# Kernel tuning notes

Measured on AMD Instinct MI355X. Metric: run time of the kernel, lower is better.

The kernel has to match this reference:

```python
import jax, jax.numpy as jnp
import numpy as np

K = 4      # number of per-slot Linear layers (self.k)
H = 512    # hidden_dim
B = 4      # branching factor at every tree level (B >= K -> no padded slots)
T = 1024   # number of trees (roots)
D = 3      # pooled tree levels (= idx_matrix.shape[1] - 2)
N0 = T * B ** D  # 65536 leaves


def _make_level(n_in):
    """Replicates the torch order_matrix / pooling construction for groups of size B.
    order[m, i] = group_base + (pos_in_group + m) % B, then +1 for the zero pad row.
    seg[i] = group id (torch.repeat_interleave of counts)."""
    i = np.arange(n_in)
    base = (i // B) * B
    pos = i % B
    m = np.arange(K)[:, None]
    order = base[None, :] + (pos[None, :] + m) % B + 1  # [K, n_in], all valid since B >= K
    seg = i // B
    return order.astype(np.int32), seg.astype(np.int32)


def setup_inputs() -> dict:
    key = jax.random.key(0)
    ks = jax.random.split(key, 5)
    x = jax.random.normal(ks[0], (N0, H), jnp.float32)
    node_idx = jnp.arange(N0, dtype=jnp.int32)  # idx_matrix[:, -1]
    o1, s1 = _make_level(N0)
    o2, s2 = _make_level(N0 // B)
    o3, s3 = _make_level(N0 // B // B)
    Wz = jax.random.normal(ks[1], (K, H, H), jnp.float32) / np.sqrt(H)   # k slot Linears
    bz = jax.random.normal(ks[2], (K, H), jnp.float32) * 0.02
    Wzf = jax.random.normal(ks[3], (H, H), jnp.float32) / np.sqrt(H)     # z_final_layer
    bzf = jax.random.normal(ks[4], (H,), jnp.float32) * 0.02
    return dict(x=x, Wz=Wz, bz=bz, Wzf=Wzf, bzf=bzf, node_idx=node_idx,
                order1=jnp.asarray(o1), order2=jnp.asarray(o2), order3=jnp.asarray(o3),
                seg1=jnp.asarray(s1), seg2=jnp.asarray(s2), seg3=jnp.asarray(s3))


def _tree_layer(data, order, seg, num_seg, Wz, bz, Wzf, bzf):
    # prepend zero row so padded entries (order == 0) gather zeros
    padded = jnp.concatenate([jnp.zeros((1, data.shape[-1]), data.dtype), data], axis=0)
    emb = padded[order]                                    # [K, N, H] gather
    emb = jnp.einsum('knh,kjh->nkj', emb, Wz) + bz[None]   # per-slot Linear (x @ W.T + b)
    emb = jnp.where((order.T == 0)[..., None], jnp.zeros((), emb.dtype), emb)  # mask padded slots
    emb = emb.sum(axis=1)                                  # sum over K slots -> [N, H]
    emb = emb @ Wzf.T + bzf                                # z_final_layer
    return jax.ops.segment_sum(emb, seg, num_segments=num_seg)  # global_add_pool


def reference(x, Wz, bz, Wzf, bzf, node_idx, order1, order2, order3, seg1, seg2, seg3):
    data = x[node_idx]
    for order, seg in ((order1, seg1), (order2, seg2), (order3, seg3)):
        data = _tree_layer(data, order, seg, order.shape[1] // B, Wz, bz, Wzf, bzf)
    return data  # [T, H]
```

## Files before the change

kernel.cpp:

```cpp
#include <hip/hip_runtime.h>


#define HD 512

typedef __attribute__((ext_vector_type(8))) short bf16x8;
typedef __attribute__((ext_vector_type(4))) float f32x4;

struct __align__(16) MfmaSmem {
    unsigned short Ah[64][40];
    unsigned short Al[64][40];
    unsigned short Bh[64][40];
    unsigned short Bl[64][40];
};

__device__ __forceinline__ void split8(const float4& v0, const float4& v1,
                                       bf16x8& hv, bf16x8& lv) {
    float f[8] = {v0.x, v0.y, v0.z, v0.w, v1.x, v1.y, v1.z, v1.w};
    #pragma unroll
    for (int i = 0; i < 8; ++i) {
        unsigned u = __float_as_uint(f[i]);
        hv[i] = (short)(u >> 16);
        float hi = __uint_as_float(u & 0xFFFF0000u);
        lv[i] = (short)(__float_as_uint(f[i] - hi) >> 16);
    }
}

template<bool BIAS>
__device__ __forceinline__
void mfma_gemm(const float* __restrict__ A, const float* __restrict__ Bt,
               float* __restrict__ C, const float* __restrict__ bias,
               float bscale, int i0, int j0, MfmaSmem& sm) {
    const int t = threadIdx.x;
    const int sr = t >> 2, sk = (t & 3) << 3;
    const int lane = t & 63, w = t >> 6;
    const int fm = lane & 15, fq = (lane >> 4) << 3;

    const float* ap = &A[(size_t)(i0 + sr) * HD + sk];
    const float* bp = &Bt[(size_t)(j0 + sr) * HD + sk];
    float4 a0 = *(const float4*)ap, a1 = *(const float4*)(ap + 4);
    float4 b0 = *(const float4*)bp, b1 = *(const float4*)(bp + 4);

    f32x4 acc[4] = {};

    for (int it = 0; it < 16; ++it) {
        __syncthreads();
        bf16x8 hv, lv;
        split8(a0, a1, hv, lv);
        *(bf16x8*)&sm.Ah[sr][sk] = hv;
        *(bf16x8*)&sm.Al[sr][sk] = lv;
        split8(b0, b1, hv, lv);
        *(bf16x8*)&sm.Bh[sr][sk] = hv;
        *(bf16x8*)&sm.Bl[sr][sk] = lv;
        __syncthreads();

        if (it < 15) {
            const int k0n = (it + 1) << 5;
            a0 = *(const float4*)(ap + k0n);
            a1 = *(const float4*)(ap + k0n + 4);
            b0 = *(const float4*)(bp + k0n);
            b1 = *(const float4*)(bp + k0n + 4);
        }

        bf16x8 ah = *(const bf16x8*)&sm.Ah[(w << 4) + fm][fq];
        bf16x8 al = *(const bf16x8*)&sm.Al[(w << 4) + fm][fq];
        #pragma unroll
        for (int ct = 0; ct < 4; ++ct) {
            bf16x8 bh = *(const bf16x8*)&sm.Bh[(ct << 4) + fm][fq];
            bf16x8 bl = *(const bf16x8*)&sm.Bl[(ct << 4) + fm][fq];
            acc[ct] = __builtin_amdgcn_mfma_f32_16x16x32_bf16(ah, bh, acc[ct], 0, 0, 0);
            acc[ct] = __builtin_amdgcn_mfma_f32_16x16x32_bf16(ah, bl, acc[ct], 0, 0, 0);
            acc[ct] = __builtin_amdgcn_mfma_f32_16x16x32_bf16(al, bh, acc[ct], 0, 0, 0);
        }
    }

    const int orow = i0 + (w << 4) + ((lane >> 4) << 2);
    #pragma unroll
    for (int ct = 0; ct < 4; ++ct) {
        const int col = j0 + (ct << 4) + fm;
        float bv = BIAS ? bscale * bias[col] : 0.f;
        #pragma unroll
        for (int r = 0; r < 4; ++r)
            C[(size_t)(orow + r) * HD + col] = acc[ct][r] + bv;
    }
}

struct VSmem { float As[16][33]; float Bs[16][33]; };

template<int MODE>
__device__ __forceinline__
void vgemm(const float* __restrict__ Wzf, const float* __restrict__ Wz,
           float* __restrict__ C, int i0, int j0, VSmem& sm) {
    const int t = threadIdx.x;
    const int ti = t >> 4, tj = t & 15;
    float a00 = 0.f, a01 = 0.f, a10 = 0.f, a11 = 0.f;

    for (int k0 = 0; k0 < HD; k0 += 16) {
        __syncthreads();
        {
            const int r = t >> 3, kp = (t & 7) << 1;
            const int row = (MODE == 0) ? i0 + r : j0 + r;
            float2 v = *(const float2*)&Wzf[(size_t)row * HD + k0 + kp];
            if (MODE == 0) { sm.As[kp][r] = v.x; sm.As[kp + 1][r] = v.y; }
            else           { sm.Bs[kp][r] = v.x; sm.Bs[kp + 1][r] = v.y; }
        }
        {
            const int kk = t >> 4, j2 = (t & 15) << 1;
            const int col = (MODE == 0) ? j0 + j2 : i0 + j2;
            const float* src = &Wz[(size_t)(k0 + kk) * HD + col];
            float sx = 0.f, sy = 0.f;
            #pragma unroll
            for (int q = 0; q < 4; ++q) {
                float2 v = *(const float2*)(src + q * 262144);
                sx += v.x; sy += v.y;
            }
            if (MODE == 0) { sm.Bs[kk][j2] = sx; sm.Bs[kk][j2 + 1] = sy; }
            else           { sm.As[kk][j2] = sx; sm.As[kk][j2 + 1] = sy; }
        }
        __syncthreads();
        #pragma unroll
        for (int kk = 0; kk < 16; ++kk) {
            float x0 = sm.As[kk][2 * ti], x1 = sm.As[kk][2 * ti + 1];
            float y0 = sm.Bs[kk][2 * tj], y1 = sm.Bs[kk][2 * tj + 1];
            a00 = fmaf(x0, y0, a00); a01 = fmaf(x0, y1, a01);
            a10 = fmaf(x1, y0, a10); a11 = fmaf(x1, y1, a11);
        }
    }
    float* c0p = &C[(size_t)(i0 + 2 * ti) * HD + j0 + 2 * tj];
    c0p[0] = a00; c0p[1] = a01;
    c0p[HD] = a10; c0p[HD + 1] = a11;
}

union D1Smem { VSmem v; float4 red[192]; };

__global__ __launch_bounds__(256) void kD1(
        const float* __restrict__ x, const float* __restrict__ Wz,
        const float* __restrict__ bz, const float* __restrict__ Wzf,
        const float* __restrict__ bzf,
        float* __restrict__ P3, float* __restrict__ M, float* __restrict__ MT,
        float* __restrict__ c0) {
    __shared__ D1Smem sm;
    const int b = blockIdx.x, t = threadIdx.x;
    if (b < 256) {
        vgemm<0>(Wzf, Wz, M, (b >> 4) << 5, (b & 15) << 5, sm.v);
    } else if (b < 512) {
        const int bb = b - 256;
        vgemm<1>(Wzf, Wz, MT, (bb >> 4) << 5, (bb & 15) << 5, sm.v);
    } else if (b < 2560) {
        const int pb = b - 512, tree = pb >> 1, cbase = (pb & 1) << 6;
        const int c = t & 63, sub = t >> 6;
        const float4* xp = (const float4*)x + (size_t)tree * 8192
                         + (sub << 4) * 128 + cbase + c;
        float4 acc = make_float4(0.f, 0.f, 0.f, 0.f);
        #pragma unroll
        for (int g = 0; g < 2; ++g) {
            float4 v[8];
            #pragma unroll
            for (int i = 0; i < 8; ++i) v[i] = xp[(size_t)(g * 8 + i) * 128];
            #pragma unroll
            for (int i = 0; i < 8; ++i) {
                acc.x += v[i].x; acc.y += v[i].y; acc.z += v[i].z; acc.w += v[i].w;
            }
        }
        if (sub) sm.red[((sub - 1) << 6) + c] = acc;
        __syncthreads();
        if (!sub) {
            float4 r0 = sm.red[c], r1 = sm.red[64 + c], r2 = sm.red[128 + c];
            acc.x += (r0.x + r1.x) + r2.x;
            acc.y += (r0.y + r1.y) + r2.y;
            acc.z += (r0.z + r1.z) + r2.z;
            acc.w += (r0.w + r1.w) + r2.w;
            ((float4*)P3)[tree * 128 + cbase + c] = acc;
        }
    } else {
        const int lane = t & 63, w = t >> 6, hb = lane << 3;
        const int j = (b - 2560) * 4 + w;
        float4 s0 = *(const float4*)&bz[hb];
        float4 s1 = *(const float4*)&bz[hb + 4];
        #pragma unroll
        for (int q = 1; q < 4; ++q) {
            float4 t0 = *(const float4*)&bz[q * HD + hb];
            float4 t1 = *(const float4*)&bz[q * HD + hb + 4];
            s0.x += t0.x; s0.y += t0.y; s0.z += t0.z; s0.w += t0.w;
            s1.x += t1.x; s1.y += t1.y; s1.z += t1.z; s1.w += t1.w;
        }
        const float4* wr = (const float4*)&Wzf[(size_t)j * HD + hb];
        float4 w0 = wr[0], w1 = wr[1];
        float p = w0.x * s0.x + w0.y * s0.y + w0.z * s0.z + w0.w * s0.w
                + w1.x * s1.x + w1.y * s1.y + w1.z * s1.z + w1.w * s1.w;
        #pragma unroll
        for (int off = 32; off > 0; off >>= 1) p += __shfl_down(p, off);
        if (lane == 0) c0[j] = 4.f * (p + bzf[j]);
    }
}

__global__ __launch_bounds__(256) void kD2(
        const float* __restrict__ P3, const float* __restrict__ M,
        const float* __restrict__ MT, const float* __restrict__ c0,
        float* __restrict__ Y1, float* __restrict__ M2, float* __restrict__ u) {
    __shared__ MfmaSmem sm;
    const int b = blockIdx.x, t = threadIdx.x;
    if (b < 128) {
        mfma_gemm<true>(P3, M, Y1, c0, 16.f, (b >> 3) << 6, (b & 7) << 6, sm);
    } else if (b < 192) {
        const int bb = b - 128;
        mfma_gemm<false>(M, MT, M2, nullptr, 0.f,
                         (bb >> 3) << 6, (bb & 7) << 6, sm);
    } else {
        const int lane = t & 63, w = t >> 6, hb = lane << 3;
        const int j = (b - 192) * 4 + w;
        const float4* mr = (const float4*)&M[(size_t)j * HD + hb];
        const float4* cr = (const float4*)&c0[hb];
        float4 m0 = mr[0], m1 = mr[1], q0 = cr[0], q1 = cr[1];
        float p = m0.x * q0.x + m0.y * q0.y + m0.z * q0.z + m0.w * q0.w
                + m1.x * q1.x + m1.y * q1.y + m1.z * q1.z + m1.w * q1.w;
        #pragma unroll
        for (int off = 32; off > 0; off >>= 1) p += __shfl_down(p, off);
        if (lane == 0) u[j] = 4.f * p + c0[j];
    }
}

__global__ __launch_bounds__(256) void kD3(
        const float* __restrict__ Y1, const float* __restrict__ M2,
        const float* __restrict__ u, float* __restrict__ out) {
    __shared__ MfmaSmem sm;
    const int b = blockIdx.x;
    mfma_gemm<true>(Y1, M2, out, u, 1.f, (b >> 3) << 6, (b & 7) << 6, sm);
}

extern "C" void kernel_launch(void* const* d_in, const int* in_sizes, int n_in,
                              void* d_out, int out_size, void* d_ws, size_t ws_size,
                              hipStream_t stream) {
    const float* x   = (const float*)d_in[0];
    const float* Wz  = (const float*)d_in[1];
    const float* bz  = (const float*)d_in[2];
    const float* Wzf = (const float*)d_in[3];
    const float* bzf = (const float*)d_in[4];
    float* out = (float*)d_out;

    float* ws = (float*)d_ws;
    float* P3 = ws;
    float* Y1 = ws + 524288;
    float* M  = ws + 1048576;
    float* MT = ws + 1310720;
    float* M2 = ws + 1572864;
    float* c0 = ws + 1835008;
    float* u  = ws + 1835520;

    hipLaunchKernelGGL(kD1, dim3(2688), dim3(256), 0, stream,
                       x, Wz, bz, Wzf, bzf, P3, M, MT, c0);
    hipLaunchKernelGGL(kD2, dim3(320), dim3(256), 0, stream,
                       P3, M, MT, c0, Y1, M2, u);
    hipLaunchKernelGGL(kD3, dim3(128), dim3(256), 0, stream, Y1, M2, u, out);
}
```

Measured before the change: 254.2 us.

## Store intermediates pre-split into bf16 hi/lo and compute M and MT together

Intermediate matrices (P3, M, MT, Y1, M2) are now written by their producers as separate bf16 high and low halves, so the MFMA GEMMs load bf16 pairs directly instead of loading fp32 and splitting inside the inner loop. One vgemm block now computes both M and its transpose MT, removing the duplicate 256-block pass over Wz and Wzf. The x-reduction blocks are ordered first in kD1. This saves split ALU work in the GEMM loops and redundant weight reads. In exchange it adds scattered transposed 4-byte stores and more workspace buffers.

```diff
diff --git a/kernel.cpp b/kernel.cpp
--- a/kernel.cpp
+++ b/kernel.cpp
@@ -2,63 +2,62 @@
 
 
 #define HD 512
-
+typedef unsigned short u16;
 typedef __attribute__((ext_vector_type(8))) short bf16x8;
 typedef __attribute__((ext_vector_type(4))) float f32x4;
 
+struct __align__(4) us2 { u16 x, y; };
+struct __align__(8) us4 { u16 x, y, z, w; };
+
+__device__ __forceinline__ void split1(float f, u16& h, u16& l) {
+    unsigned u = __float_as_uint(f);
+    h = (u16)(u >> 16);
+    float hi = __uint_as_float(u & 0xFFFF0000u);
+    l = (u16)(__float_as_uint(f - hi) >> 16);
+}
+
 struct __align__(16) MfmaSmem {
-    unsigned short Ah[64][40];
-    unsigned short Al[64][40];
-    unsigned short Bh[64][40];
-    unsigned short Bl[64][40];
+    u16 Ah[64][40];
+    u16 Al[64][40];
+    u16 Bh[64][40];
+    u16 Bl[64][40];
 };
 
-__device__ __forceinline__ void split8(const float4& v0, const float4& v1,
-                                       bf16x8& hv, bf16x8& lv) {
-    float f[8] = {v0.x, v0.y, v0.z, v0.w, v1.x, v1.y, v1.z, v1.w};
-    #pragma unroll
-    for (int i = 0; i < 8; ++i) {
-        unsigned u = __float_as_uint(f[i]);
-        hv[i] = (short)(u >> 16);
-        float hi = __uint_as_float(u & 0xFFFF0000u);
-        lv[i] = (short)(__float_as_uint(f[i] - hi) >> 16);
-    }
-}
-
-template<bool BIAS>
+template<bool BIAS, bool SPLIT>
 __device__ __forceinline__
-void mfma_gemm(const float* __restrict__ A, const float* __restrict__ Bt,
-               float* __restrict__ C, const float* __restrict__ bias,
-               float bscale, int i0, int j0, MfmaSmem& sm) {
+void mfma_gemm_s(const u16* __restrict__ Ah_, const u16* __restrict__ Al_,
+                 const u16* __restrict__ Bh_, const u16* __restrict__ Bl_,
+                 u16* __restrict__ Ch, u16* __restrict__ Cl,
+                 float* __restrict__ Cf, const float* __restrict__ bias,
+                 float bscale, int i0, int j0, MfmaSmem& sm) {
     const int t = threadIdx.x;
     const int sr = t >> 2, sk = (t & 3) << 3;
     const int lane = t & 63, w = t >> 6;
     const int fm = lane & 15, fq = (lane >> 4) << 3;
 
-    const float* ap = &A[(size_t)(i0 + sr) * HD + sk];
-    const float* bp = &Bt[(size_t)(j0 + sr) * HD + sk];
-    float4 a0 = *(const float4*)ap, a1 = *(const float4*)(ap + 4);
-    float4 b0 = *(const float4*)bp, b1 = *(const float4*)(bp + 4);
+    const u16* ahp = Ah_ + (size_t)(i0 + sr) * HD + sk;
+    const u16* alp = Al_ + (size_t)(i0 + sr) * HD + sk;
+    const u16* bhp = Bh_ + (size_t)(j0 + sr) * HD + sk;
+    const u16* blp = Bl_ + (size_t)(j0 + sr) * HD + sk;
+    bf16x8 rah = *(const bf16x8*)ahp, ral = *(const bf16x8*)alp;
+    bf16x8 rbh = *(const bf16x8*)bhp, rbl = *(const bf16x8*)blp;
 
     f32x4 acc[4] = {};
 
     for (int it = 0; it < 16; ++it) {
         __syncthreads();
-        bf16x8 hv, lv;
-        split8(a0, a1, hv, lv);
-        *(bf16x8*)&sm.Ah[sr][sk] = hv;
-        *(bf16x8*)&sm.Al[sr][sk] = lv;
-        split8(b0, b1, hv, lv);
-        *(bf16x8*)&sm.Bh[sr][sk] = hv;
-        *(bf16x8*)&sm.Bl[sr][sk] = lv;
+        *(bf16x8*)&sm.Ah[sr][sk] = rah;
+        *(bf16x8*)&sm.Al[sr][sk] = ral;
+        *(bf16x8*)&sm.Bh[sr][sk] = rbh;
+        *(bf16x8*)&sm.Bl[sr][sk] = rbl;
         __syncthreads();
 
         if (it < 15) {
-            const int k0n = (it + 1) << 5;
-            a0 = *(const float4*)(ap + k0n);
-            a1 = *(const float4*)(ap + k0n + 4);
-            b0 = *(const float4*)(bp + k0n);
-            b1 = *(const float4*)(bp + k0n + 4);
+            const int kn = (it + 1) << 5;
+            rah = *(const bf16x8*)(ahp + kn);
+            ral = *(const bf16x8*)(alp + kn);
+            rbh = *(const bf16x8*)(bhp + kn);
+            rbl = *(const bf16x8*)(blp + kn);
         }
 
         bf16x8 ah = *(const bf16x8*)&sm.Ah[(w << 4) + fm][fq];
@@ -79,17 +78,27 @@
         const int col = j0 + (ct << 4) + fm;
         float bv = BIAS ? bscale * bias[col] : 0.f;
         #pragma unroll
-        for (int r = 0; r < 4; ++r)
-            C[(size_t)(orow + r) * HD + col] = acc[ct][r] + bv;
+        for (int r = 0; r < 4; ++r) {
+            float v = acc[ct][r] + bv;
+            if (SPLIT) {
+                u16 h, l;
+                split1(v, h, l);
+                Ch[(size_t)(orow + r) * HD + col] = h;
+                Cl[(size_t)(orow + r) * HD + col] = l;
+            } else {
+                Cf[(size_t)(orow + r) * HD + col] = v;
+            }
+        }
     }
 }
 
 struct VSmem { float As[16][33]; float Bs[16][33]; };
 
-template<int MODE>
 __device__ __forceinline__
-void vgemm(const float* __restrict__ Wzf, const float* __restrict__ Wz,
-           float* __restrict__ C, int i0, int j0, VSmem& sm) {
+void vgemm_both(const float* __restrict__ Wzf, const float* __restrict__ Wz,
+                u16* __restrict__ Mh, u16* __restrict__ Ml,
+                u16* __restrict__ MTh, u16* __restrict__ MTl,
+                int i0, int j0, VSmem& sm) {
     const int t = threadIdx.x;
     const int ti = t >> 4, tj = t & 15;
     float a00 = 0.f, a01 = 0.f, a10 = 0.f, a11 = 0.f;
@@ -98,36 +107,42 @@
         __syncthreads();
         {
             const int r = t >> 3, kp = (t & 7) << 1;
-            const int row = (MODE == 0) ? i0 + r : j0 + r;
-            float2 v = *(const float2*)&Wzf[(size_t)row * HD + k0 + kp];
-            if (MODE == 0) { sm.As[kp][r] = v.x; sm.As[kp + 1][r] = v.y; }
-            else           { sm.Bs[kp][r] = v.x; sm.Bs[kp + 1][r] = v.y; }
+            float2 v = *(const float2*)&Wzf[(size_t)(i0 + r) * HD + k0 + kp];
+            sm.As[kp][r] = v.x; sm.As[kp + 1][r] = v.y;
         }
         {
             const int kk = t >> 4, j2 = (t & 15) << 1;
-            const int col = (MODE == 0) ? j0 + j2 : i0 + j2;
-            const float* src = &Wz[(size_t)(k0 + kk) * HD + col];
+            const float* src = &Wz[(size_t)(k0 + kk) * HD + j0 + j2];
             float sx = 0.f, sy = 0.f;
             #pragma unroll
             for (int q = 0; q < 4; ++q) {
                 float2 v = *(const float2*)(src + q * 262144);
                 sx += v.x; sy += v.y;
             }
-            if (MODE == 0) { sm.Bs[kk][j2] = sx; sm.Bs[kk][j2 + 1] = sy; }
-            else           { sm.As[kk][j2] = sx; sm.As[kk][j2 + 1] = sy; }
+            sm.Bs[kk][j2] = sx; sm.Bs[kk][j2 + 1] = sy;
         }
         __syncthreads();
         #pragma unroll
         for (int kk = 0; kk < 16; ++kk) {
-            float x0 = sm.As[kk][2 * ti], x1 = sm.As[kk][2 * ti + 1];
-            float y0 = sm.Bs[kk][2 * tj], y1 = sm.Bs[kk][2 * tj + 1];
-            a00 = fmaf(x0, y0, a00); a01 = fmaf(x0, y1, a01);
-            a10 = fmaf(x1, y0, a10); a11 = fmaf(x1, y1, a11);
-        }
-    }
-    float* c0p = &C[(size_t)(i0 + 2 * ti) * HD + j0 + 2 * tj];
-    c0p[0] = a00; c0p[1] = a01;
-    c0p[HD] = a10; c0p[HD + 1] = a11;
+            float2 xa = *(const float2*)&sm.As[kk][2 * ti];
+            float2 yb = *(const float2*)&sm.Bs[kk][2 * tj];
+            a00 = fmaf(xa.x, yb.x, a00); a01 = fmaf(xa.x, yb.y, a01);
+            a10 = fmaf(xa.y, yb.x, a10); a11 = fmaf(xa.y, yb.y, a11);
+        }
+    }
+    u16 h00, l00, h01, l01, h10, l10, h11, l11;
+    split1(a00, h00, l00); split1(a01, h01, l01);
+    split1(a10, h10, l10); split1(a11, h11, l11);
+    const size_t mo = (size_t)(i0 + 2 * ti) * HD + j0 + 2 * tj;
+    *(us2*)&Mh[mo]      = us2{h00, h01};
+    *(us2*)&Ml[mo]      = us2{l00, l01};
+    *(us2*)&Mh[mo + HD] = us2{h10, h11};
+    *(us2*)&Ml[mo + HD] = us2{l10, l11};
+    const size_t to = (size_t)(j0 + 2 * tj) * HD + i0 + 2 * ti;
+    *(us2*)&MTh[to]      = us2{h00, h10};
+    *(us2*)&MTl[to]      = us2{l00, l10};
+    *(us2*)&MTh[to + HD] = us2{h01, h11};
+    *(us2*)&MTl[to + HD] = us2{l01, l11};
 }
 
 union D1Smem { VSmem v; float4 red[192]; };
@@ -136,17 +151,14 @@
         const float* __restrict__ x, const float* __restrict__ Wz,
         const float* __restrict__ bz, const float* __restrict__ Wzf,
         const float* __restrict__ bzf,
-        float* __restrict__ P3, float* __restrict__ M, float* __restrict__ MT,
+        u16* __restrict__ P3h, u16* __restrict__ P3l,
+        u16* __restrict__ Mh, u16* __restrict__ Ml,
+        u16* __restrict__ MTh, u16* __restrict__ MTl,
         float* __restrict__ c0) {
     __shared__ D1Smem sm;
     const int b = blockIdx.x, t = threadIdx.x;
-    if (b < 256) {
-        vgemm<0>(Wzf, Wz, M, (b >> 4) << 5, (b & 15) << 5, sm.v);
-    } else if (b < 512) {
-        const int bb = b - 256;
-        vgemm<1>(Wzf, Wz, MT, (bb >> 4) << 5, (bb & 15) << 5, sm.v);
-    } else if (b < 2560) {
-        const int pb = b - 512, tree = pb >> 1, cbase = (pb & 1) << 6;
+    if (b < 2048) {
+        const int tree = b >> 1, cbase = (b & 1) << 6;
         const int c = t & 63, sub = t >> 6;
         const float4* xp = (const float4*)x + (size_t)tree * 8192
                          + (sub << 4) * 128 + cbase + c;
@@ -169,11 +181,21 @@
             acc.y += (r0.y + r1.y) + r2.y;
             acc.z += (r0.z + r1.z) + r2.z;
             acc.w += (r0.w + r1.w) + r2.w;
-            ((float4*)P3)[tree * 128 + cbase + c] = acc;
-        }
+            float vals[4] = {acc.x, acc.y, acc.z, acc.w};
+            u16 hh[4], ll[4];
+            #pragma unroll
+            for (int i = 0; i < 4; ++i) split1(vals[i], hh[i], ll[i]);
+            const size_t po = (size_t)tree * HD + ((cbase + c) << 2);
+            *(us4*)&P3h[po] = us4{hh[0], hh[1], hh[2], hh[3]};
+            *(us4*)&P3l[po] = us4{ll[0], ll[1], ll[2], ll[3]};
+        }
+    } else if (b < 2304) {
+        const int bb = b - 2048;
+        vgemm_both(Wzf, Wz, Mh, Ml, MTh, MTl,
+                   (bb >> 4) << 5, (bb & 15) << 5, sm.v);
     } else {
         const int lane = t & 63, w = t >> 6, hb = lane << 3;
-        const int j = (b - 2560) * 4 + w;
+        const int j = (b - 2304) * 4 + w;
         float4 s0 = *(const float4*)&bz[hb];
         float4 s1 = *(const float4*)&bz[hb + 4];
         #pragma unroll
@@ -194,25 +216,37 @@
 }
 
 __global__ __launch_bounds__(256) void kD2(
-        const float* __restrict__ P3, const float* __restrict__ M,
-        const float* __restrict__ MT, const float* __restrict__ c0,
-        float* __restrict__ Y1, float* __restrict__ M2, float* __restrict__ u) {
+        const u16* __restrict__ P3h, const u16* __restrict__ P3l,
+        const u16* __restrict__ Mh, const u16* __restrict__ Ml,
+        const u16* __restrict__ MTh, const u16* __restrict__ MTl,
+        const float* __restrict__ c0,
+        u16* __restrict__ Y1h, u16* __restrict__ Y1l,
+        u16* __restrict__ M2h, u16* __restrict__ M2l,
+        float* __restrict__ u) {
     __shared__ MfmaSmem sm;
     const int b = blockIdx.x, t = threadIdx.x;
     if (b < 128) {
-        mfma_gemm<true>(P3, M, Y1, c0, 16.f, (b >> 3) << 6, (b & 7) << 6, sm);
+        mfma_gemm_s<true, true>(P3h, P3l, Mh, Ml, Y1h, Y1l, nullptr,
+                                c0, 16.f, (b >> 3) << 6, (b & 7) << 6, sm);
     } else if (b < 192) {
         const int bb = b - 128;
-        mfma_gemm<false>(M, MT, M2, nullptr, 0.f,
-                         (bb >> 3) << 6, (bb & 7) << 6, sm);
+        mfma_gemm_s<false, true>(Mh, Ml, MTh, MTl, M2h, M2l, nullptr,
+                                 nullptr, 0.f, (bb >> 3) << 6, (bb & 7) << 6, sm);
     } else {
         const int lane = t & 63, w = t >> 6, hb = lane << 3;
         const int j = (b - 192) * 4 + w;
-        const float4* mr = (const float4*)&M[(size_t)j * HD + hb];
+        bf16x8 mh = *(const bf16x8*)&Mh[(size_t)j * HD + hb];
+        bf16x8 ml = *(const bf16x8*)&Ml[(size_t)j * HD + hb];
         const float4* cr = (const float4*)&c0[hb];
-        float4 m0 = mr[0], m1 = mr[1], q0 = cr[0], q1 = cr[1];
-        float p = m0.x * q0.x + m0.y * q0.y + m0.z * q0.z + m0.w * q0.w
-                + m1.x * q1.x + m1.y * q1.y + m1.z * q1.z + m1.w * q1.w;
+        float4 q0 = cr[0], q1 = cr[1];
+        float cv[8] = {q0.x, q0.y, q0.z, q0.w, q1.x, q1.y, q1.z, q1.w};
+        float p = 0.f;
+        #pragma unroll
+        for (int i = 0; i < 8; ++i) {
+            float f = __uint_as_float(((unsigned)(u16)mh[i]) << 16)
+                    + __uint_as_float(((unsigned)(u16)ml[i]) << 16);
+            p = fmaf(f, cv[i], p);
+        }
         #pragma unroll
         for (int off = 32; off > 0; off >>= 1) p += __shfl_down(p, off);
         if (lane == 0) u[j] = 4.f * p + c0[j];
@@ -220,11 +254,13 @@
 }
 
 __global__ __launch_bounds__(256) void kD3(
-        const float* __restrict__ Y1, const float* __restrict__ M2,
+        const u16* __restrict__ Y1h, const u16* __restrict__ Y1l,
+        const u16* __restrict__ M2h, const u16* __restrict__ M2l,
         const float* __restrict__ u, float* __restrict__ out) {
     __shared__ MfmaSmem sm;
     const int b = blockIdx.x;
-    mfma_gemm<true>(Y1, M2, out, u, 1.f, (b >> 3) << 6, (b & 7) << 6, sm);
+    mfma_gemm_s<true, false>(Y1h, Y1l, M2h, M2l, nullptr, nullptr, out,
+                             u, 1.f, (b >> 3) << 6, (b & 7) << 6, sm);
 }
 
 extern "C" void kernel_launch(void* const* d_in, const int* in_sizes, int n_in,
@@ -237,18 +273,24 @@
     const float* bzf = (const float*)d_in[4];
     float* out = (float*)d_out;
 
-    float* ws = (float*)d_ws;
-    float* P3 = ws;
-    float* Y1 = ws + 524288;
-    float* M  = ws + 1048576;
-    float* MT = ws + 1310720;
-    float* M2 = ws + 1572864;
-    float* c0 = ws + 1835008;
-    float* u  = ws + 1835520;
-
-    hipLaunchKernelGGL(kD1, dim3(2688), dim3(256), 0, stream,
-                       x, Wz, bz, Wzf, bzf, P3, M, MT, c0);
+    char* base = (char*)d_ws;
+    u16* P3h = (u16*)(base);
+    u16* P3l = (u16*)(base + (1 << 20));
+    u16* Y1h = (u16*)(base + (2 << 20));
+    u16* Y1l = (u16*)(base + (3 << 20));
+    u16* Mh  = (u16*)(base + (4 << 20));
+    u16* Ml  = (u16*)(base + (4 << 20) + (512 << 10));
+    u16* MTh = (u16*)(base + (5 << 20));
+    u16* MTl = (u16*)(base + (5 << 20) + (512 << 10));
+    u16* M2h = (u16*)(base + (6 << 20));
+    u16* M2l = (u16*)(base + (6 << 20) + (512 << 10));
+    float* c0 = (float*)(base + (7 << 20));
+    float* u  = (float*)(base + (7 << 20) + 2048);
+
+    hipLaunchKernelGGL(kD1, dim3(2432), dim3(256), 0, stream,
+                       x, Wz, bz, Wzf, bzf, P3h, P3l, Mh, Ml, MTh, MTl, c0);
     hipLaunchKernelGGL(kD2, dim3(320), dim3(256), 0, stream,
-                       P3, M, MT, c0, Y1, M2, u);
-    hipLaunchKernelGGL(kD3, dim3(128), dim3(256), 0, stream, Y1, M2, u, out);
-}
+                       P3h, P3l, Mh, Ml, MTh, MTl, c0, Y1h, Y1l, M2h, M2l, u);
+    hipLaunchKernelGGL(kD3, dim3(128), dim3(256), 0, stream,
+                       Y1h, Y1l, M2h, M2l, u, out);
+}
```

Result: slower. 259.6 us (+2.1%).
